# Optimization experiments

Measured on AMD Instinct MI355X. Metric: run time of the kernel, lower is better.

## Reference

```python
import jax, jax.numpy as jnp
import numpy as np

MIN_NORM = 1e-15
BALL_EPS = 4e-3   # float32 boundary eps (HGCN PoincareBall convention)
ATANH_EPS = 1e-7  # artanh clamp margin safe in fp32 (orig 1e-15 in fp64)
C = 1.0           # curvature


def _norm(x):
    return jnp.clip(jnp.linalg.norm(x, axis=-1, keepdims=True), MIN_NORM, None)


def artanh(x):
    x = jnp.clip(x, -1.0 + ATANH_EPS, 1.0 - ATANH_EPS)
    return 0.5 * (jnp.log1p(x) - jnp.log1p(-x))


def proj(x, c):
    norm = _norm(x)
    maxnorm = (1.0 - BALL_EPS) / jnp.sqrt(c)
    return jnp.where(norm > maxnorm, x / norm * maxnorm, x)


def expmap0(u, c):
    sqrt_c = jnp.sqrt(c)
    u_norm = _norm(u)
    return jnp.tanh(sqrt_c * u_norm) * u / (sqrt_c * u_norm)


def logmap0(p, c):
    sqrt_c = jnp.sqrt(c)
    p_norm = _norm(p)
    return artanh(sqrt_c * p_norm) * p / (sqrt_c * p_norm)


def mobius_add(x, y, c):
    x2 = jnp.sum(x * x, axis=-1, keepdims=True)
    y2 = jnp.sum(y * y, axis=-1, keepdims=True)
    xy = jnp.sum(x * y, axis=-1, keepdims=True)
    num = (1.0 + 2.0 * c * xy + c * y2) * x + (1.0 - c * x2) * y
    denom = 1.0 + 2.0 * c * xy + c * c * x2 * y2
    return num / jnp.clip(denom, MIN_NORM, None)


def mobius_matvec(W, x, c):
    # W: [out, in], x: [N, in]
    sqrt_c = jnp.sqrt(c)
    x_norm = _norm(x)
    mx = x @ W.T                      # [N, out]
    mx_norm = _norm(mx)
    res_c = jnp.tanh(mx_norm / x_norm * artanh(sqrt_c * x_norm)) * mx / (mx_norm * sqrt_c)
    cond = jnp.all(mx == 0.0, axis=-1, keepdims=True)
    return jnp.where(cond, 0.0, res_c)


def setup_inputs() -> dict:
    key = jax.random.key(0)
    k1, k2 = jax.random.split(key)
    N, din, dout = 524288, 128, 128
    # points on the Poincare ball: expmap0 of small tangent vectors
    u = 0.1 * jax.random.normal(k1, (N, din), dtype=jnp.float32)
    x = proj(expmap0(u, C), C)
    # xavier_uniform with gain=sqrt(2)
    bound = np.sqrt(2.0) * np.sqrt(6.0 / (din + dout))
    W = jax.random.uniform(k2, (dout, din), dtype=jnp.float32, minval=-bound, maxval=bound)
    b = jnp.zeros((dout,), dtype=jnp.float32)
    return {"x": x, "W": W, "b": b}


def reference(x, W, b):
    # dropout p=0 / eval -> identity on W
    res = proj(mobius_matvec(W, x, C), C)
    # proj_tan0 is identity on the Poincare ball
    hyp_bias = proj(expmap0(b[None, :], C), C)
    res = proj(mobius_add(res, hyp_bias, C), C)
    # nonlinearity in tangent space at origin
    res = jax.nn.relu(logmap0(res, C))
    res = proj(expmap0(res, C), C)
    return res
```

## Files before the change

### kernel.cpp

```cpp
#include <hip/hip_runtime.h>

typedef __attribute__((ext_vector_type(8))) short short8;
typedef __attribute__((ext_vector_type(4))) float f32x4;

#define MAXNORM 0.996f
#define MINNORM 1e-15f
#define ATEPS   (1.0f - 1e-7f)

__device__ __forceinline__ float frcp(float x) { return __builtin_amdgcn_rcpf(x); }
__device__ __forceinline__ float artanh_c(float z) {
    z = fminf(z, ATEPS);
    return 0.5f * __logf((1.0f + z) * frcp(1.0f - z));
}
__device__ __forceinline__ float tanh_pos(float a) {
    float e = __expf(-2.0f * a);
    return (1.0f - e) * frcp(1.0f + e);
}
__device__ __forceinline__ unsigned short f2bf(float f) {
    union { float f; unsigned u; } v; v.f = f;
    unsigned r = v.u + 0x7FFFu + ((v.u >> 16) & 1u);
    return (unsigned short)(r >> 16);
}

__global__ __launch_bounds__(256) void blinear_kernel(
    const float* __restrict__ Xf,
    const float* __restrict__ Wf,
    const float* __restrict__ Bf,
    float* __restrict__ Out)
{
    const int lane = threadIdx.x & 63;
    const int wave = threadIdx.x >> 6;
    const int c = lane & 15;
    const int q = lane >> 4;
    const long rowbase = (long)blockIdx.x * 128 + wave * 32;

    float b0 = Bf[lane];
    float b1 = Bf[64 + lane];
    float bn2 = b0 * b0 + b1 * b1;
    #pragma unroll
    for (int m = 1; m <= 32; m <<= 1) bn2 += __shfl_xor(bn2, m);
    float bn = fmaxf(sqrtf(bn2), MINNORM);
    float tb = tanh_pos(bn);
    float fb = fminf(tb, MAXNORM) * frcp(bn);
    float hb2 = fb * fb * bn2;
    float hbv[8];
    #pragma unroll
    for (int nt = 0; nt < 8; ++nt) hbv[nt] = fb * Bf[nt * 16 + c];

    short8 afr[2][4];
    float xq[2] = {0.0f, 0.0f};
    #pragma unroll
    for (int t = 0; t < 2; ++t) {
        const float* xrow = Xf + (rowbase + t * 16 + c) * 128;
        #pragma unroll
        for (int ks = 0; ks < 4; ++ks) {
            f32x4 a0 = *(const f32x4*)(xrow + ks * 32 + q * 8);
            f32x4 a1 = *(const f32x4*)(xrow + ks * 32 + q * 8 + 4);
            short8 s;
            #pragma unroll
            for (int j = 0; j < 4; ++j) {
                float v0 = a0[j], v1 = a1[j];
                xq[t] = fmaf(v0, v0, fmaf(v1, v1, xq[t]));
                s[j] = (short)f2bf(v0);
                s[4 + j] = (short)f2bf(v1);
            }
            afr[t][ks] = s;
        }
    }
    #pragma unroll
    for (int t = 0; t < 2; ++t) { xq[t] += __shfl_xor(xq[t], 16); xq[t] += __shfl_xor(xq[t], 32); }
    float xn2v[2][4];
    #pragma unroll
    for (int t = 0; t < 2; ++t)
        #pragma unroll
        for (int r = 0; r < 4; ++r) xn2v[t][r] = __shfl(xq[t], q * 4 + r);

    f32x4 acc[2][8];
    {
        f32x4 z = {0.0f, 0.0f, 0.0f, 0.0f};
        #pragma unroll
        for (int t = 0; t < 2; ++t)
            #pragma unroll
            for (int nt = 0; nt < 8; ++nt) acc[t][nt] = z;
    }
    #pragma unroll
    for (int nt = 0; nt < 8; ++nt) {
        const float* wrow = Wf + (nt * 16 + c) * 128;
        #pragma unroll
        for (int ks = 0; ks < 4; ++ks) {
            f32x4 w0 = *(const f32x4*)(wrow + ks * 32 + q * 8);
            f32x4 w1 = *(const f32x4*)(wrow + ks * 32 + q * 8 + 4);
            short8 bfr;
            #pragma unroll
            for (int j = 0; j < 4; ++j) {
                bfr[j] = (short)f2bf(w0[j]);
                bfr[4 + j] = (short)f2bf(w1[j]);
            }
            acc[0][nt] = __builtin_amdgcn_mfma_f32_16x16x32_bf16(afr[0][ks], bfr, acc[0][nt], 0, 0, 0);
            acc[1][nt] = __builtin_amdgcn_mfma_f32_16x16x32_bf16(afr[1][ks], bfr, acc[1][nt], 0, 0, 0);
        }
    }

    float mn2[2][4] = {}, mhb[2][4] = {};
    #pragma unroll
    for (int t = 0; t < 2; ++t)
        #pragma unroll
        for (int nt = 0; nt < 8; ++nt)
            #pragma unroll
            for (int r = 0; r < 4; ++r) {
                float v = acc[t][nt][r];
                mn2[t][r] = fmaf(v, v, mn2[t][r]);
                mhb[t][r] = fmaf(v, hbv[nt], mhb[t][r]);
            }
    #pragma unroll
    for (int m = 1; m <= 8; m <<= 1)
        #pragma unroll
        for (int t = 0; t < 2; ++t)
            #pragma unroll
            for (int r = 0; r < 4; ++r) {
                mn2[t][r] += __shfl_xor(mn2[t][r], m);
                mhb[t][r] += __shfl_xor(mhb[t][r], m);
            }

    float A1[2][4], B1[2][4], Gg[2][4], S3[2][4];
    #pragma unroll
    for (int t = 0; t < 2; ++t)
        #pragma unroll
        for (int r = 0; r < 4; ++r) {
            float xn = fmaxf(sqrtf(xn2v[t][r]), MINNORM);
            float mn = fmaxf(sqrtf(mn2[t][r]), MINNORM);
            float t1 = tanh_pos(mn * frcp(xn) * artanh_c(xn));
            float rn = fminf(t1, MAXNORM);
            float f1 = rn * frcp(mn);
            float x2 = rn * rn;
            float xy = f1 * mhb[t][r];
            float Aa = 1.0f + 2.0f * xy + hb2;
            float Bb = 1.0f - x2;
            float Dn = fmaxf(1.0f + 2.0f * xy + x2 * hb2, MINNORM);
            float rD = frcp(Dn);
            float a1 = Aa * f1 * rD;
            float b1_ = Bb * rD;
            float r2n2 = a1 * a1 * mn2[t][r] + 2.0f * a1 * b1_ * mhb[t][r] + b1_ * b1_ * hb2;
            float r2n = sqrtf(fmaxf(r2n2, 0.0f));
            float g = (r2n > MAXNORM) ? (MAXNORM * frcp(r2n)) : 1.0f;
            float n3 = fmaxf(fminf(r2n, MAXNORM), MINNORM);
            float s3 = artanh_c(n3) * frcp(n3);
            A1[t][r] = a1; B1[t][r] = b1_; Gg[t][r] = g; S3[t][r] = s3;
        }

    float q2[2][4] = {};
    #pragma unroll
    for (int t = 0; t < 2; ++t)
        #pragma unroll
        for (int nt = 0; nt < 8; ++nt)
            #pragma unroll
            for (int r = 0; r < 4; ++r) {
                float v = fmaf(A1[t][r], acc[t][nt][r], B1[t][r] * hbv[nt]);
                v = fmaxf(v, 0.0f);
                acc[t][nt][r] = v;
                q2[t][r] = fmaf(v, v, q2[t][r]);
            }
    #pragma unroll
    for (int m = 1; m <= 8; m <<= 1)
        #pragma unroll
        for (int t = 0; t < 2; ++t)
            #pragma unroll
            for (int r = 0; r < 4; ++r) q2[t][r] += __shfl_xor(q2[t][r], m);

    float K[2][4];
    #pragma unroll
    for (int t = 0; t < 2; ++t)
        #pragma unroll
        for (int r = 0; r < 4; ++r) {
            float sg = S3[t][r] * Gg[t][r];
            float tn_t = sg * sqrtf(q2[t][r]);
            float tn = fmaxf(tn_t, MINNORM);
            float t4 = tanh_pos(tn);
            K[t][r] = fminf(t4, MAXNORM) * frcp(tn) * sg;
        }

    #pragma unroll
    for (int t = 0; t < 2; ++t)
        #pragma unroll
        for (int r = 0; r < 4; ++r) {
            long row = rowbase + t * 16 + q * 4 + r;
            float* orow = Out + row * 128;
            #pragma unroll
            for (int nt = 0; nt < 8; ++nt)
                orow[nt * 16 + c] = K[t][r] * acc[t][nt][r];
        }
}

extern "C" void kernel_launch(void* const* d_in, const int* in_sizes, int n_in,
                              void* d_out, int out_size, void* d_ws, size_t ws_size,
                              hipStream_t stream) {
    const float* X = (const float*)d_in[0];
    const float* W = (const float*)d_in[1];
    const float* B = (const float*)d_in[2];
    float* Out = (float*)d_out;
    const int N = in_sizes[0] / 128;
    const int blocks = N / 128;
    blinear_kernel<<<blocks, 256, 0, stream>>>(X, W, B, Out);
}
```

Before: 514.4 us.

## Prepack W to bf16 MFMA fragments, halve rows per wave, use nontemporal stores

A small pre-kernel converts W to bf16 and lays it out in MFMA B-fragment order in the workspace, so each wave loads ready short8 fragments instead of loading fp32 W and converting it. Each wave now handles 16 rows instead of 32, which doubles the grid size and cuts register pressure, but W fragments are reused across half as many rows. Output stores become nontemporal so the streaming output does not pollute the cache. The extra launch adds a little fixed overhead, and W is prepacked on every call, not cached.

```diff
diff --git a/kernel.cpp b/kernel.cpp
--- a/kernel.cpp
+++ b/kernel.cpp
@@ -22,9 +22,27 @@
     return (unsigned short)(r >> 16);
 }
 
+__global__ __launch_bounds__(256) void wpack_kernel(
+    const float* __restrict__ Wf, short8* __restrict__ Wp)
+{
+    const int tid = blockIdx.x * 256 + threadIdx.x;
+    const int l = tid & 63;
+    const int f = tid >> 6;
+    const int nt = f >> 2, ks = f & 3;
+    const int c = l & 15, q = l >> 4;
+    const float* src = Wf + (nt * 16 + c) * 128 + ks * 32 + q * 8;
+    short8 s;
+    #pragma unroll
+    for (int j = 0; j < 4; ++j) {
+        s[j]     = (short)f2bf(src[j]);
+        s[4 + j] = (short)f2bf(src[4 + j]);
+    }
+    Wp[tid] = s;
+}
+
 __global__ __launch_bounds__(256) void blinear_kernel(
     const float* __restrict__ Xf,
-    const float* __restrict__ Wf,
+    const short8* __restrict__ Wp,
     const float* __restrict__ Bf,
     float* __restrict__ Out)
 {
@@ -32,7 +50,7 @@
     const int wave = threadIdx.x >> 6;
     const int c = lane & 15;
     const int q = lane >> 4;
-    const long rowbase = (long)blockIdx.x * 128 + wave * 32;
+    const long rowbase = (long)blockIdx.x * 64 + wave * 16;
 
     float b0 = Bf[lane];
     float b1 = Bf[64 + lane];
@@ -47,148 +65,118 @@
     #pragma unroll
     for (int nt = 0; nt < 8; ++nt) hbv[nt] = fb * Bf[nt * 16 + c];
 
-    short8 afr[2][4];
-    float xq[2] = {0.0f, 0.0f};
+    short8 afr[4];
+    float xq = 0.0f;
+    const float* xrow = Xf + (rowbase + c) * 128;
     #pragma unroll
-    for (int t = 0; t < 2; ++t) {
-        const float* xrow = Xf + (rowbase + t * 16 + c) * 128;
+    for (int ks = 0; ks < 4; ++ks) {
+        f32x4 a0 = *(const f32x4*)(xrow + ks * 32 + q * 8);
+        f32x4 a1 = *(const f32x4*)(xrow + ks * 32 + q * 8 + 4);
+        short8 s;
         #pragma unroll
-        for (int ks = 0; ks < 4; ++ks) {
-            f32x4 a0 = *(const f32x4*)(xrow + ks * 32 + q * 8);
-            f32x4 a1 = *(const f32x4*)(xrow + ks * 32 + q * 8 + 4);
-            short8 s;
-            #pragma unroll
-            for (int j = 0; j < 4; ++j) {
-                float v0 = a0[j], v1 = a1[j];
-                xq[t] = fmaf(v0, v0, fmaf(v1, v1, xq[t]));
-                s[j] = (short)f2bf(v0);
-                s[4 + j] = (short)f2bf(v1);
-            }
-            afr[t][ks] = s;
+        for (int j = 0; j < 4; ++j) {
+            float v0 = a0[j], v1 = a1[j];
+            xq = fmaf(v0, v0, fmaf(v1, v1, xq));
+            s[j] = (short)f2bf(v0);
+            s[4 + j] = (short)f2bf(v1);
         }
+        afr[ks] = s;
     }
+    xq += __shfl_xor(xq, 16);
+    xq += __shfl_xor(xq, 32);
+    float xn2v[4];
     #pragma unroll
-    for (int t = 0; t < 2; ++t) { xq[t] += __shfl_xor(xq[t], 16); xq[t] += __shfl_xor(xq[t], 32); }
-    float xn2v[2][4];
-    #pragma unroll
-    for (int t = 0; t < 2; ++t)
-        #pragma unroll
-        for (int r = 0; r < 4; ++r) xn2v[t][r] = __shfl(xq[t], q * 4 + r);
+    for (int r = 0; r < 4; ++r) xn2v[r] = __shfl(xq, q * 4 + r);
 
-    f32x4 acc[2][8];
+    f32x4 acc[8];
     {
         f32x4 z = {0.0f, 0.0f, 0.0f, 0.0f};
         #pragma unroll
-        for (int t = 0; t < 2; ++t)
-            #pragma unroll
-            for (int nt = 0; nt < 8; ++nt) acc[t][nt] = z;
+        for (int nt = 0; nt < 8; ++nt) acc[nt] = z;
     }
     #pragma unroll
     for (int nt = 0; nt < 8; ++nt) {
-        const float* wrow = Wf + (nt * 16 + c) * 128;
         #pragma unroll
         for (int ks = 0; ks < 4; ++ks) {
-            f32x4 w0 = *(const f32x4*)(wrow + ks * 32 + q * 8);
-            f32x4 w1 = *(const f32x4*)(wrow + ks * 32 + q * 8 + 4);
-            short8 bfr;
-            #pragma unroll
-            for (int j = 0; j < 4; ++j) {
-                bfr[j] = (short)f2bf(w0[j]);
-                bfr[4 + j] = (short)f2bf(w1[j]);
-            }
-            acc[0][nt] = __builtin_amdgcn_mfma_f32_16x16x32_bf16(afr[0][ks], bfr, acc[0][nt], 0, 0, 0);
-            acc[1][nt] = __builtin_amdgcn_mfma_f32_16x16x32_bf16(afr[1][ks], bfr, acc[1][nt], 0, 0, 0);
+            short8 bfr = Wp[(nt * 4 + ks) * 64 + lane];
+            acc[nt] = __builtin_amdgcn_mfma_f32_16x16x32_bf16(afr[ks], bfr, acc[nt], 0, 0, 0);
         }
     }
 
-    float mn2[2][4] = {}, mhb[2][4] = {};
+    float mn2[4] = {}, mhb[4] = {};
     #pragma unroll
-    for (int t = 0; t < 2; ++t)
+    for (int nt = 0; nt < 8; ++nt)
         #pragma unroll
-        for (int nt = 0; nt < 8; ++nt)
-            #pragma unroll
-            for (int r = 0; r < 4; ++r) {
-                float v = acc[t][nt][r];
-                mn2[t][r] = fmaf(v, v, mn2[t][r]);
-                mhb[t][r] = fmaf(v, hbv[nt], mhb[t][r]);
-            }
+        for (int r = 0; r < 4; ++r) {
+            float v = acc[nt][r];
+            mn2[r] = fmaf(v, v, mn2[r]);
+            mhb[r] = fmaf(v, hbv[nt], mhb[r]);
+        }
     #pragma unroll
     for (int m = 1; m <= 8; m <<= 1)
         #pragma unroll
-        for (int t = 0; t < 2; ++t)
-            #pragma unroll
-            for (int r = 0; r < 4; ++r) {
-                mn2[t][r] += __shfl_xor(mn2[t][r], m);
-                mhb[t][r] += __shfl_xor(mhb[t][r], m);
-            }
+        for (int r = 0; r < 4; ++r) {
+            mn2[r] += __shfl_xor(mn2[r], m);
+            mhb[r] += __shfl_xor(mhb[r], m);
+        }
 
-    float A1[2][4], B1[2][4], Gg[2][4], S3[2][4];
+    float A1[4], B1[4], Gg[4], S3[4];
     #pragma unroll
-    for (int t = 0; t < 2; ++t)
+    for (int r = 0; r < 4; ++r) {
+        float xn = fmaxf(sqrtf(xn2v[r]), MINNORM);
+        float mn = fmaxf(sqrtf(mn2[r]), MINNORM);
+        float t1 = tanh_pos(mn * frcp(xn) * artanh_c(xn));
+        float rn = fminf(t1, MAXNORM);
+        float f1 = rn * frcp(mn);
+        float x2 = rn * rn;
+        float xy = f1 * mhb[r];
+        float Aa = 1.0f + 2.0f * xy + hb2;
+        float Bb = 1.0f - x2;
+        float Dn = fmaxf(1.0f + 2.0f * xy + x2 * hb2, MINNORM);
+        float rD = frcp(Dn);
+        float a1 = Aa * f1 * rD;
+        float b1_ = Bb * rD;
+        float r2n2 = a1 * a1 * mn2[r] + 2.0f * a1 * b1_ * mhb[r] + b1_ * b1_ * hb2;
+        float r2n = sqrtf(fmaxf(r2n2, 0.0f));
+        float g = (r2n > MAXNORM) ? (MAXNORM * frcp(r2n)) : 1.0f;
+        float n3 = fmaxf(fminf(r2n, MAXNORM), MINNORM);
+        float s3 = artanh_c(n3) * frcp(n3);
+        A1[r] = a1; B1[r] = b1_; Gg[r] = g; S3[r] = s3;
+    }
+
+    float q2[4] = {};
+    #pragma unroll
+    for (int nt = 0; nt < 8; ++nt)
         #pragma unroll
         for (int r = 0; r < 4; ++r) {
-            float xn = fmaxf(sqrtf(xn2v[t][r]), MINNORM);
-            float mn = fmaxf(sqrtf(mn2[t][r]), MINNORM);
-            float t1 = tanh_pos(mn * frcp(xn) * artanh_c(xn));
-            float rn = fminf(t1, MAXNORM);
-            float f1 = rn * frcp(mn);
-            float x2 = rn * rn;
-            float xy = f1 * mhb[t][r];
-            float Aa = 1.0f + 2.0f * xy + hb2;
-            float Bb = 1.0f - x2;
-            float Dn = fmaxf(1.0f + 2.0f * xy + x2 * hb2, MINNORM);
-            float rD = frcp(Dn);
-            float a1 = Aa * f1 * rD;
-            float b1_ = Bb * rD;
-            float r2n2 = a1 * a1 * mn2[t][r] + 2.0f * a1 * b1_ * mhb[t][r] + b1_ * b1_ * hb2;
-            float r2n = sqrtf(fmaxf(r2n2, 0.0f));
-            float g = (r2n > MAXNORM) ? (MAXNORM * frcp(r2n)) : 1.0f;
-            float n3 = fmaxf(fminf(r2n, MAXNORM), MINNORM);
-            float s3 = artanh_c(n3) * frcp(n3);
-            A1[t][r] = a1; B1[t][r] = b1_; Gg[t][r] = g; S3[t][r] = s3;
+            float v = fmaf(A1[r], acc[nt][r], B1[r] * hbv[nt]);
+            v = fmaxf(v, 0.0f);
+            acc[nt][r] = v;
+            q2[r] = fmaf(v, v, q2[r]);
         }
-
-    float q2[2][4] = {};
-    #pragma unroll
-    for (int t = 0; t < 2; ++t)
-        #pragma unroll
-        for (int nt = 0; nt < 8; ++nt)
-            #pragma unroll
-            for (int r = 0; r < 4; ++r) {
-                float v = fmaf(A1[t][r], acc[t][nt][r], B1[t][r] * hbv[nt]);
-                v = fmaxf(v, 0.0f);
-                acc[t][nt][r] = v;
-                q2[t][r] = fmaf(v, v, q2[t][r]);
-            }
     #pragma unroll
     for (int m = 1; m <= 8; m <<= 1)
         #pragma unroll
-        for (int t = 0; t < 2; ++t)
-            #pragma unroll
-            for (int r = 0; r < 4; ++r) q2[t][r] += __shfl_xor(q2[t][r], m);
+        for (int r = 0; r < 4; ++r) q2[r] += __shfl_xor(q2[r], m);
 
-    float K[2][4];
+    float K[4];
     #pragma unroll
-    for (int t = 0; t < 2; ++t)
-        #pragma unroll
-        for (int r = 0; r < 4; ++r) {
-            float sg = S3[t][r] * Gg[t][r];
-            float tn_t = sg * sqrtf(q2[t][r]);
-            float tn = fmaxf(tn_t, MINNORM);
-            float t4 = tanh_pos(tn);
-            K[t][r] = fminf(t4, MAXNORM) * frcp(tn) * sg;
-        }
+    for (int r = 0; r < 4; ++r) {
+        float sg = S3[r] * Gg[r];
+        float tn_t = sg * sqrtf(q2[r]);
+        float tn = fmaxf(tn_t, MINNORM);
+        float t4 = tanh_pos(tn);
+        K[r] = fminf(t4, MAXNORM) * frcp(tn) * sg;
+    }
 
     #pragma unroll
-    for (int t = 0; t < 2; ++t)
+    for (int r = 0; r < 4; ++r) {
+        long row = rowbase + q * 4 + r;
+        float* orow = Out + row * 128;
         #pragma unroll
-        for (int r = 0; r < 4; ++r) {
-            long row = rowbase + t * 16 + q * 4 + r;
-            float* orow = Out + row * 128;
-            #pragma unroll
-            for (int nt = 0; nt < 8; ++nt)
-                orow[nt * 16 + c] = K[t][r] * acc[t][nt][r];
-        }
+        for (int nt = 0; nt < 8; ++nt)
+            __builtin_nontemporal_store(K[r] * acc[nt][r], orow + nt * 16 + c);
+    }
 }
 
 extern "C" void kernel_launch(void* const* d_in, const int* in_sizes, int n_in,
@@ -198,7 +186,8 @@
     const float* W = (const float*)d_in[1];
     const float* B = (const float*)d_in[2];
     float* Out = (float*)d_out;
+    short8* Wp = (short8*)d_ws;
     const int N = in_sizes[0] / 128;
-    const int blocks = N / 128;
-    blinear_kernel<<<blocks, 256, 0, stream>>>(X, W, B, Out);
+    wpack_kernel<<<8, 256, 0, stream>>>(W, Wp);
+    blinear_kernel<<<N / 64, 256, 0, stream>>>(X, Wp, B, Out);
 }
```

Measured after the change: 459.8 us. 10.6% less time.
